# Performance work log

Hardware: AMD Instinct MI355X
Metric: run time of the kernel (lower is better)

The kernel has to match this reference:

```python
import jax, jax.numpy as jnp
import numpy as np

B, N, D = 32, 1024, 256

def setup_inputs() -> dict:
    key = jax.random.key(0)
    ks = jax.random.split(key, 7)
    s = 1.0 / np.sqrt(D)
    return {
        "traj": jax.random.normal(ks[0], (B, N, D), dtype=jnp.float32),
        "Wq": jax.random.normal(ks[1], (D, D), dtype=jnp.float32) * s,
        "bq": jax.random.normal(ks[2], (D,), dtype=jnp.float32) * s,
        "Wk": jax.random.normal(ks[3], (D, D), dtype=jnp.float32) * s,
        "bk": jax.random.normal(ks[4], (D,), dtype=jnp.float32) * s,
        "Wv": jax.random.normal(ks[5], (D, D), dtype=jnp.float32) * s,
        "bv": jax.random.normal(ks[6], (D,), dtype=jnp.float32) * s,
    }

def reference(traj, Wq, bq, Wk, bk, Wv, bv):
    # torch nn.Linear: y = x @ W.T + b
    q = jnp.einsum('bnd,ed->bne', traj, Wq) + bq  # [B,N,D]
    k = jnp.einsum('bnd,ed->bne', traj, Wk) + bk  # [B,N,D]
    v = jnp.einsum('bnd,ed->bne', traj, Wv) + bv  # [B,N,D]
    # unscaled dot-product attention (original sums broadcasted Q*K over D)
    scores = jnp.einsum('bnd,bmd->bnm', q, k)     # [B,N,N]
    attn = jax.nn.softmax(scores, axis=-1)        # [B,N,N]
    out = jnp.einsum('bnm,bmd->bnd', attn, v)     # [B,N,D]
    return out
```

## Files before the change

### kernel.cpp

```cpp
#include <hip/hip_runtime.h>

#define NN 1024
#define DD 256

typedef __attribute__((ext_vector_type(8))) _Float16 f16x8;
typedef __attribute__((ext_vector_type(4))) _Float16 f16x4;
typedef __attribute__((ext_vector_type(4))) float f32x4;

union H8 { f16x8 v; _Float16 s[8]; };

__device__ __forceinline__ void g2lds16(const void* g, void* l) {
  __builtin_amdgcn_global_load_lds(
      (const __attribute__((address_space(1))) void*)g,
      (__attribute__((address_space(3))) void*)l, 16, 0, 0);
}

__global__ void wconv_kernel(const float* __restrict__ Wq, const float* __restrict__ Wk,
                             const float* __restrict__ Wv, _Float16* __restrict__ pw) {
  int c = blockIdx.x * 256 + threadIdx.x;
  int lane = c & 63;
  int nt = (c >> 6) & 1;
  int kk = (c >> 7) & 7;
  int et = c >> 10;
  int e = et * 32 + nt * 16 + (lane & 15);
  int d = kk * 32 + (lane >> 4) * 8;
  const float* W = (e < 256) ? Wq : (e < 512 ? Wk : Wv);
  const float* src = W + (e & 255) * 256 + d;
  H8 xx;
  for (int j = 0; j < 8; ++j) xx.s[j] = (_Float16)src[j];
  *(f16x8*)(pw + (size_t)c * 8) = xx.v;
}

__global__ __launch_bounds__(256, 2) void proj_kernel(
    const float* __restrict__ traj,
    const float* __restrict__ bq, const float* __restrict__ bk, const float* __restrict__ bv,
    const _Float16* __restrict__ pw,
    _Float16* __restrict__ pq, _Float16* __restrict__ pk, _Float16* __restrict__ pv)
{
  __shared__ alignas(16) _Float16 Wl[2][8192];
  __shared__ alignas(16) _Float16 Cs[4][1280];

  const int t = threadIdx.x;
  const int lane = t & 63, wave = t >> 6;
  const int col16 = lane & 15, quad = lane >> 4;
  const int mt = blockIdx.x >> 1, eh = blockIdx.x & 1;
  const int mbase = mt * 128;
  const int bb = mbase >> 10;

  f16x8 aq[2][8];
  for (int s = 0; s < 2; ++s) {
    const float* ap = traj + (size_t)(mbase + wave * 32 + s * 16 + col16) * DD;
    for (int kk = 0; kk < 8; ++kk) {
      float4 u0 = *(const float4*)(ap + kk * 32 + quad * 8);
      float4 u1 = *(const float4*)(ap + kk * 32 + quad * 8 + 4);
      H8 xx;
      xx.s[0] = (_Float16)u0.x; xx.s[1] = (_Float16)u0.y;
      xx.s[2] = (_Float16)u0.z; xx.s[3] = (_Float16)u0.w;
      xx.s[4] = (_Float16)u1.x; xx.s[5] = (_Float16)u1.y;
      xx.s[6] = (_Float16)u1.z; xx.s[7] = (_Float16)u1.w;
      aq[s][kk] = xx.v;
    }
  }

  const f32x4 zero = {0.f, 0.f, 0.f, 0.f};
  const int et0 = eh * 12;

  for (int i = 0; i < 4; ++i)
    g2lds16(pw + (size_t)et0 * 8192 + (size_t)(i * 256 + t) * 8, Wl[0] + (i * 256 + t) * 8);
  for (int i = 0; i < 4; ++i)
    g2lds16(pw + (size_t)(et0 + 1) * 8192 + (size_t)(i * 256 + t) * 8, Wl[1] + (i * 256 + t) * 8);

  for (int ei = 0; ei < 12; ++ei) {
    if (ei == 0)      asm volatile("s_waitcnt vmcnt(4)" ::: "memory");
    else if (ei < 11) asm volatile("s_waitcnt vmcnt(6)" ::: "memory");
    else              asm volatile("s_waitcnt vmcnt(0)" ::: "memory");
    __builtin_amdgcn_s_barrier();
    asm volatile("" ::: "memory");

    const _Float16* wl = Wl[ei & 1];

    f32x4 acc[2][2];
    acc[0][0] = zero; acc[0][1] = zero; acc[1][0] = zero; acc[1][1] = zero;
    for (int kk = 0; kk < 8; ++kk)
      for (int nt = 0; nt < 2; ++nt) {
        f16x8 bw = *(const f16x8*)&wl[((kk * 2 + nt) * 64 + lane) * 8];
        acc[0][nt] = __builtin_amdgcn_mfma_f32_16x16x32_f16(aq[0][kk], bw, acc[0][nt], 0, 0, 0);
        acc[1][nt] = __builtin_amdgcn_mfma_f32_16x16x32_f16(aq[1][kk], bw, acc[1][nt], 0, 0, 0);
      }

    int e0 = eh * 384 + ei * 32;
    int sel = e0 >> 8;
    const float* bias = (sel == 0) ? bq : (sel == 1 ? bk : bv);
    for (int nt = 0; nt < 2; ++nt) {
      float bvl = bias[(e0 & 255) + nt * 16 + col16];
      for (int s = 0; s < 2; ++s) {
        acc[s][nt][0] += bvl; acc[s][nt][1] += bvl;
        acc[s][nt][2] += bvl; acc[s][nt][3] += bvl;
      }
    }

    _Float16* cs = Cs[wave];
    if (sel < 2) {
      for (int s = 0; s < 2; ++s)
        for (int nt = 0; nt < 2; ++nt)
          for (int r = 0; r < 4; ++r)
            cs[(s * 16 + quad * 4 + r) * 40 + nt * 16 + col16] = (_Float16)acc[s][nt][r];
      if (sel == 0) {
        for (int s = 0; s < 2; ++s) {
          f16x8 val = *(const f16x8*)&cs[(s * 16 + col16) * 40 + quad * 8];
          int g = (mbase >> 4) + wave * 2 + s;
          *(f16x8*)(pq + (size_t)((g * 8 + ei) * 64 + lane) * 8) = val;
        }
      } else {
        int kkg = (e0 - 256) >> 5;
        for (int s = 0; s < 2; ++s) {
          f16x8 val = *(const f16x8*)&cs[(s * 16 + col16) * 40 + quad * 8];
          int kgg = ((mbase & 1023) >> 4) + wave * 2 + s;
          *(f16x8*)(pk + (size_t)(((bb * 64 + kgg) * 8 + kkg) * 64 + lane) * 8) = val;
        }
      }
    } else {
      for (int s = 0; s < 2; ++s)
        for (int nt = 0; nt < 2; ++nt)
          for (int r = 0; r < 4; ++r)
            cs[(nt * 16 + col16) * 40 + s * 16 + quad * 4 + r] = (_Float16)acc[s][nt][r];
      int kt32 = ((mbase & 1023) >> 5) + wave;
      for (int dtl = 0; dtl < 2; ++dtl) {
        const _Float16* base = &cs[(dtl * 16 + col16) * 40];
        H8 val;
        *(f16x4*)&val.s[0] = *(const f16x4*)&base[quad * 4];
        *(f16x4*)&val.s[4] = *(const f16x4*)&base[16 + quad * 4];
        int dtg = ((e0 - 512) >> 4) + dtl;
        *(f16x8*)(pv + (size_t)(((bb * 32 + kt32) * 16 + dtg) * 64 + lane) * 8) = val.v;
      }
    }

    asm volatile("" ::: "memory");
    __builtin_amdgcn_s_barrier();
    if (ei < 10) {
      const _Float16* ws = pw + (size_t)(et0 + ei + 2) * 8192;
      _Float16* wd = Wl[ei & 1];
      for (int i = 0; i < 4; ++i)
        g2lds16(ws + (size_t)(i * 256 + t) * 8, wd + (i * 256 + t) * 8);
    }
  }
}

__global__ __launch_bounds__(256, 2) void attn_kernel(
    const _Float16* __restrict__ pq, const _Float16* __restrict__ pk,
    const _Float16* __restrict__ pv, float* __restrict__ out)
{
  __shared__ alignas(16) _Float16 Ks[2][8192];
  __shared__ alignas(16) _Float16 Vs[2][8192];

  const int t = threadIdx.x;
  const int lane = t & 63, wave = t >> 6;
  const int col16 = lane & 15, quad = lane >> 4;
  const int b = blockIdx.x, qt = blockIdx.y;
  const int qrow0 = b * NN + qt * 64;

  f16x8 aq[8];
  {
    int g = b * 64 + qt * 4 + wave;
#pragma unroll
    for (int kk = 0; kk < 8; ++kk)
      aq[kk] = *(const f16x8*)(pq + (size_t)((g * 8 + kk) * 64 + lane) * 8);
  }

  float m_i = -3.0e38f, l_i = 0.f;
  f32x4 O[16];
  const f32x4 zero = {0.f, 0.f, 0.f, 0.f};
#pragma unroll
  for (int dt = 0; dt < 16; ++dt) O[dt] = zero;

  const _Float16* kbb = pk + (size_t)b * 64 * 8 * 64 * 8;
  const _Float16* vbb = pv + (size_t)b * 32 * 16 * 64 * 8;

#pragma unroll
  for (int i = 0; i < 4; ++i) g2lds16(kbb + (size_t)(i * 256 + t) * 8, &Ks[0][(i * 256 + t) * 8]);
#pragma unroll
  for (int i = 0; i < 4; ++i) g2lds16(vbb + (size_t)(i * 256 + t) * 8, &Vs[0][(i * 256 + t) * 8]);
#pragma unroll
  for (int i = 0; i < 4; ++i) g2lds16(kbb + 8192 + (size_t)(i * 256 + t) * 8, &Ks[1][(i * 256 + t) * 8]);
#pragma unroll
  for (int i = 0; i < 4; ++i) g2lds16(vbb + 8192 + (size_t)(i * 256 + t) * 8, &Vs[1][(i * 256 + t) * 8]);

  for (int kt = 0; kt < 32; ++kt) {
    if (kt < 31) asm volatile("s_waitcnt vmcnt(8)" ::: "memory");
    else         asm volatile("s_waitcnt vmcnt(0)" ::: "memory");
    __builtin_amdgcn_s_barrier();
    asm volatile("" ::: "memory");

    const _Float16* ks = Ks[kt & 1];
    f32x4 S[2]; S[0] = zero; S[1] = zero;
    __builtin_amdgcn_s_setprio(1);
#pragma unroll
    for (int kk = 0; kk < 8; ++kk)
#pragma unroll
      for (int nt = 0; nt < 2; ++nt) {
        f16x8 bk_ = *(const f16x8*)&ks[((nt * 8 + kk) * 64 + lane) * 8];
        S[nt] = __builtin_amdgcn_mfma_f32_16x16x32_f16(bk_, aq[kk], S[nt], 0, 0, 0);
      }
    __builtin_amdgcn_s_setprio(0);

    float sv[8];
#pragma unroll
    for (int nt = 0; nt < 2; ++nt)
#pragma unroll
      for (int r = 0; r < 4; ++r) sv[nt * 4 + r] = S[nt][r];
    float vmax = sv[0];
#pragma unroll
    for (int j = 1; j < 8; ++j) vmax = fmaxf(vmax, sv[j]);
    vmax = fmaxf(vmax, __shfl_xor(vmax, 16));
    vmax = fmaxf(vmax, __shfl_xor(vmax, 32));

    if (__ballot(vmax > m_i + 8.0f)) {
      float nm = fmaxf(m_i, vmax);
      float alpha = __expf(m_i - nm);
      float a4[4];
#pragma unroll
      for (int r = 0; r < 4; ++r) a4[r] = __shfl(alpha, quad * 4 + r);
#pragma unroll
      for (int dt = 0; dt < 16; ++dt)
#pragma unroll
        for (int r = 0; r < 4; ++r) O[dt][r] *= a4[r];
      l_i *= alpha;
      m_i = nm;
    }
    float rs = 0.f;
    H8 px;
#pragma unroll
    for (int j = 0; j < 8; ++j) {
      float pj = __expf(sv[j] - m_i);
      rs += pj;
      px.s[j] = (_Float16)pj;
    }
    rs += __shfl_xor(rs, 16);
    rs += __shfl_xor(rs, 32);
    l_i += rs;
    f16x8 ap = px.v;

    const _Float16* vs = Vs[kt & 1];
    __builtin_amdgcn_s_setprio(1);
#pragma unroll
    for (int dt = 0; dt < 16; ++dt) {
      f16x8 bv_ = *(const f16x8*)&vs[(dt * 64 + lane) * 8];
      O[dt] = __builtin_amdgcn_mfma_f32_16x16x32_f16(ap, bv_, O[dt], 0, 0, 0);
    }
    __builtin_amdgcn_s_setprio(0);

    asm volatile("" ::: "memory");
    __builtin_amdgcn_s_barrier();
    if (kt < 30) {
      const _Float16* kg = kbb + (size_t)(kt + 2) * 8192;
      const _Float16* vg = vbb + (size_t)(kt + 2) * 8192;
      _Float16* kd = Ks[kt & 1];
      _Float16* vd = Vs[kt & 1];
#pragma unroll
      for (int i = 0; i < 4; ++i) g2lds16(kg + (size_t)(i * 256 + t) * 8, kd + (i * 256 + t) * 8);
#pragma unroll
      for (int i = 0; i < 4; ++i) g2lds16(vg + (size_t)(i * 256 + t) * 8, vd + (i * 256 + t) * 8);
    }
  }

  float linv[4];
#pragma unroll
  for (int r = 0; r < 4; ++r) linv[r] = 1.0f / __shfl(l_i, quad * 4 + r);
#pragma unroll
  for (int r = 0; r < 4; ++r) {
    float* orow = out + (size_t)(qrow0 + wave * 16 + quad * 4 + r) * DD;
#pragma unroll
    for (int dt = 0; dt < 16; ++dt)
      orow[dt * 16 + col16] = O[dt][r] * linv[r];
  }
}

extern "C" void kernel_launch(void* const* d_in, const int* in_sizes, int n_in,
                              void* d_out, int out_size, void* d_ws, size_t ws_size,
                              hipStream_t stream) {
  const float* traj = (const float*)d_in[0];
  const float* Wq   = (const float*)d_in[1];
  const float* bq   = (const float*)d_in[2];
  const float* Wk   = (const float*)d_in[3];
  const float* bk   = (const float*)d_in[4];
  const float* Wv   = (const float*)d_in[5];
  const float* bv   = (const float*)d_in[6];

  _Float16* pq = (_Float16*)d_ws;
  _Float16* pk = pq + (size_t)32768 * 256;
  _Float16* pv = pk + (size_t)32768 * 256;
  _Float16* pw = pv + (size_t)32768 * 256;

  wconv_kernel<<<96, 256, 0, stream>>>(Wq, Wk, Wv, pw);
  proj_kernel<<<512, 256, 0, stream>>>(traj, bq, bk, bv, pw, pq, pk, pv);
  attn_kernel<<<dim3(32, 16), 256, 0, stream>>>(pq, pk, pv, (float*)d_out);
}
```

Measured before the change: 165.0 us.

## Software-pipeline QK^T one tile ahead of softmax and PV in attention loop

The main attention loop now computes the QK^T scores for tile kt while running softmax and the PV product for tile kt-1, using a prologue and an epilogue. K tiles are prefetched two tiles ahead and V tiles one tile ahead, with the vmcnt waits adjusted to match. The goal is to hide softmax latency, such as exp and cross-lane shuffles, behind independent MFMA work. The cost is extra registers for the carried score tile and more complex buffer indexing and wait counts.

```diff
diff --git a/kernel.cpp b/kernel.cpp
--- a/kernel.cpp
+++ b/kernel.cpp
@@ -182,24 +182,47 @@
   for (int i = 0; i < 4; ++i) g2lds16(vbb + (size_t)(i * 256 + t) * 8, &Vs[0][(i * 256 + t) * 8]);
 #pragma unroll
   for (int i = 0; i < 4; ++i) g2lds16(kbb + 8192 + (size_t)(i * 256 + t) * 8, &Ks[1][(i * 256 + t) * 8]);
-#pragma unroll
-  for (int i = 0; i < 4; ++i) g2lds16(vbb + 8192 + (size_t)(i * 256 + t) * 8, &Vs[1][(i * 256 + t) * 8]);
-
-  for (int kt = 0; kt < 32; ++kt) {
+
+  asm volatile("s_waitcnt vmcnt(8)" ::: "memory");
+  __builtin_amdgcn_s_barrier();
+  asm volatile("" ::: "memory");
+
+  f32x4 Sp[2]; Sp[0] = zero; Sp[1] = zero;
+  {
+    const _Float16* ks = Ks[0];
+    __builtin_amdgcn_s_setprio(1);
+#pragma unroll
+    for (int kk = 0; kk < 8; ++kk)
+#pragma unroll
+      for (int nt = 0; nt < 2; ++nt) {
+        f16x8 bk_ = *(const f16x8*)&ks[((nt * 8 + kk) * 64 + lane) * 8];
+        Sp[nt] = __builtin_amdgcn_mfma_f32_16x16x32_f16(bk_, aq[kk], Sp[nt], 0, 0, 0);
+      }
+    __builtin_amdgcn_s_setprio(0);
+  }
+
+  asm volatile("" ::: "memory");
+  __builtin_amdgcn_s_barrier();
+#pragma unroll
+  for (int i = 0; i < 4; ++i) g2lds16(kbb + 2 * 8192 + (size_t)(i * 256 + t) * 8, &Ks[0][(i * 256 + t) * 8]);
+#pragma unroll
+  for (int i = 0; i < 4; ++i) g2lds16(vbb + 1 * 8192 + (size_t)(i * 256 + t) * 8, &Vs[1][(i * 256 + t) * 8]);
+
+  for (int kt = 1; kt < 32; ++kt) {
     if (kt < 31) asm volatile("s_waitcnt vmcnt(8)" ::: "memory");
-    else         asm volatile("s_waitcnt vmcnt(0)" ::: "memory");
+    else         asm volatile("s_waitcnt vmcnt(4)" ::: "memory");
     __builtin_amdgcn_s_barrier();
     asm volatile("" ::: "memory");
 
     const _Float16* ks = Ks[kt & 1];
-    f32x4 S[2]; S[0] = zero; S[1] = zero;
+    f32x4 Sc[2]; Sc[0] = zero; Sc[1] = zero;
     __builtin_amdgcn_s_setprio(1);
 #pragma unroll
     for (int kk = 0; kk < 8; ++kk)
 #pragma unroll
       for (int nt = 0; nt < 2; ++nt) {
         f16x8 bk_ = *(const f16x8*)&ks[((nt * 8 + kk) * 64 + lane) * 8];
-        S[nt] = __builtin_amdgcn_mfma_f32_16x16x32_f16(bk_, aq[kk], S[nt], 0, 0, 0);
+        Sc[nt] = __builtin_amdgcn_mfma_f32_16x16x32_f16(bk_, aq[kk], Sc[nt], 0, 0, 0);
       }
     __builtin_amdgcn_s_setprio(0);
 
@@ -207,13 +230,12 @@
 #pragma unroll
     for (int nt = 0; nt < 2; ++nt)
 #pragma unroll
-      for (int r = 0; r < 4; ++r) sv[nt * 4 + r] = S[nt][r];
+      for (int r = 0; r < 4; ++r) sv[nt * 4 + r] = Sp[nt][r];
     float vmax = sv[0];
 #pragma unroll
     for (int j = 1; j < 8; ++j) vmax = fmaxf(vmax, sv[j]);
     vmax = fmaxf(vmax, __shfl_xor(vmax, 16));
     vmax = fmaxf(vmax, __shfl_xor(vmax, 32));
-
     if (__ballot(vmax > m_i + 8.0f)) {
       float nm = fmaxf(m_i, vmax);
       float alpha = __expf(m_i - nm);
@@ -240,7 +262,7 @@
     l_i += rs;
     f16x8 ap = px.v;
 
-    const _Float16* vs = Vs[kt & 1];
+    const _Float16* vs = Vs[(kt - 1) & 1];
     __builtin_amdgcn_s_setprio(1);
 #pragma unroll
     for (int dt = 0; dt < 16; ++dt) {
@@ -251,16 +273,68 @@
 
     asm volatile("" ::: "memory");
     __builtin_amdgcn_s_barrier();
-    if (kt < 30) {
+    if (kt <= 29) {
       const _Float16* kg = kbb + (size_t)(kt + 2) * 8192;
-      const _Float16* vg = vbb + (size_t)(kt + 2) * 8192;
       _Float16* kd = Ks[kt & 1];
-      _Float16* vd = Vs[kt & 1];
 #pragma unroll
       for (int i = 0; i < 4; ++i) g2lds16(kg + (size_t)(i * 256 + t) * 8, kd + (i * 256 + t) * 8);
+    }
+    if (kt <= 30) {
+      const _Float16* vg = vbb + (size_t)(kt + 1) * 8192;
+      _Float16* vd = Vs[(kt + 1) & 1];
 #pragma unroll
       for (int i = 0; i < 4; ++i) g2lds16(vg + (size_t)(i * 256 + t) * 8, vd + (i * 256 + t) * 8);
     }
+    Sp[0] = Sc[0]; Sp[1] = Sc[1];
+  }
+
+  asm volatile("s_waitcnt vmcnt(0)" ::: "memory");
+  __builtin_amdgcn_s_barrier();
+  asm volatile("" ::: "memory");
+  {
+    float sv[8];
+#pragma unroll
+    for (int nt = 0; nt < 2; ++nt)
+#pragma unroll
+      for (int r = 0; r < 4; ++r) sv[nt * 4 + r] = Sp[nt][r];
+    float vmax = sv[0];
+#pragma unroll
+    for (int j = 1; j < 8; ++j) vmax = fmaxf(vmax, sv[j]);
+    vmax = fmaxf(vmax, __shfl_xor(vmax, 16));
+    vmax = fmaxf(vmax, __shfl_xor(vmax, 32));
+    if (__ballot(vmax > m_i + 8.0f)) {
+      float nm = fmaxf(m_i, vmax);
+      float alpha = __expf(m_i - nm);
+      float a4[4];
+#pragma unroll
+      for (int r = 0; r < 4; ++r) a4[r] = __shfl(alpha, quad * 4 + r);
+#pragma unroll
+      for (int dt = 0; dt < 16; ++dt)
+#pragma unroll
+        for (int r = 0; r < 4; ++r) O[dt][r] *= a4[r];
+      l_i *= alpha;
+      m_i = nm;
+    }
+    float rs = 0.f;
+    H8 px;
+#pragma unroll
+    for (int j = 0; j < 8; ++j) {
+      float pj = __expf(sv[j] - m_i);
+      rs += pj;
+      px.s[j] = (_Float16)pj;
+    }
+    rs += __shfl_xor(rs, 16);
+    rs += __shfl_xor(rs, 32);
+    l_i += rs;
+    f16x8 ap = px.v;
+    const _Float16* vs = Vs[1];
+    __builtin_amdgcn_s_setprio(1);
+#pragma unroll
+    for (int dt = 0; dt < 16; ++dt) {
+      f16x8 bv_ = *(const f16x8*)&vs[(dt * 64 + lane) * 8];
+      O[dt] = __builtin_amdgcn_mfma_f32_16x16x32_f16(ap, bv_, O[dt], 0, 0, 0);
+    }
+    __builtin_amdgcn_s_setprio(0);
   }
 
   float linv[4];
```

After: 164.5 us, median of 2. Within noise of the previous version (-0.3%).

## Single-buffer V in LDS via register staging and raise occupancy bound

Applied to the files above, without the earlier changes.

The V tile is no longer double-buffered in LDS. The next V tile is loaded into registers at the top of each iteration and written to a single LDS buffer after the PV MFMAs, guarded by an extra lgkmcnt wait and barrier. This cuts LDS per block to 48KB so the launch bound can go from 2 to 3 blocks per CU. The cost is a second barrier per iteration, more live registers that cap the VGPR budget, and V loads that are no longer asynchronous. With 512 blocks on 256 CUs the extra occupancy slot may go unused.

```diff
diff --git a/kernel.cpp b/kernel.cpp
--- a/kernel.cpp
+++ b/kernel.cpp
@@ -146,12 +146,12 @@
   }
 }
 
-__global__ __launch_bounds__(256, 2) void attn_kernel(
+__global__ __launch_bounds__(256, 3) void attn_kernel(
     const _Float16* __restrict__ pq, const _Float16* __restrict__ pk,
     const _Float16* __restrict__ pv, float* __restrict__ out)
 {
   __shared__ alignas(16) _Float16 Ks[2][8192];
-  __shared__ alignas(16) _Float16 Vs[2][8192];
+  __shared__ alignas(16) _Float16 Vs[8192];
 
   const int t = threadIdx.x;
   const int lane = t & 63, wave = t >> 6;
@@ -178,18 +178,29 @@
 
 #pragma unroll
   for (int i = 0; i < 4; ++i) g2lds16(kbb + (size_t)(i * 256 + t) * 8, &Ks[0][(i * 256 + t) * 8]);
-#pragma unroll
-  for (int i = 0; i < 4; ++i) g2lds16(vbb + (size_t)(i * 256 + t) * 8, &Vs[0][(i * 256 + t) * 8]);
+  float4 vr0, vr1, vr2, vr3;
+  {
+    const float4* vgp = (const float4*)vbb;
+    vr0 = vgp[0 * 256 + t]; vr1 = vgp[1 * 256 + t];
+    vr2 = vgp[2 * 256 + t]; vr3 = vgp[3 * 256 + t];
+  }
 #pragma unroll
   for (int i = 0; i < 4; ++i) g2lds16(kbb + 8192 + (size_t)(i * 256 + t) * 8, &Ks[1][(i * 256 + t) * 8]);
-#pragma unroll
-  for (int i = 0; i < 4; ++i) g2lds16(vbb + 8192 + (size_t)(i * 256 + t) * 8, &Vs[1][(i * 256 + t) * 8]);
+  {
+    float4* vsp = (float4*)Vs;
+    vsp[0 * 256 + t] = vr0; vsp[1 * 256 + t] = vr1;
+    vsp[2 * 256 + t] = vr2; vsp[3 * 256 + t] = vr3;
+  }
+  asm volatile("s_waitcnt lgkmcnt(0)" ::: "memory");
+  __builtin_amdgcn_s_barrier();
+  asm volatile("" ::: "memory");
 
   for (int kt = 0; kt < 32; ++kt) {
-    if (kt < 31) asm volatile("s_waitcnt vmcnt(8)" ::: "memory");
-    else         asm volatile("s_waitcnt vmcnt(0)" ::: "memory");
-    __builtin_amdgcn_s_barrier();
-    asm volatile("" ::: "memory");
+    if (kt < 31) {
+      const float4* vgp = (const float4*)(vbb + (size_t)(kt + 1) * 8192);
+      vr0 = vgp[0 * 256 + t]; vr1 = vgp[1 * 256 + t];
+      vr2 = vgp[2 * 256 + t]; vr3 = vgp[3 * 256 + t];
+    }
 
     const _Float16* ks = Ks[kt & 1];
     f32x4 S[2]; S[0] = zero; S[1] = zero;
@@ -240,27 +251,32 @@
     l_i += rs;
     f16x8 ap = px.v;
 
-    const _Float16* vs = Vs[kt & 1];
     __builtin_amdgcn_s_setprio(1);
 #pragma unroll
     for (int dt = 0; dt < 16; ++dt) {
-      f16x8 bv_ = *(const f16x8*)&vs[(dt * 64 + lane) * 8];
+      f16x8 bv_ = *(const f16x8*)&Vs[(dt * 64 + lane) * 8];
       O[dt] = __builtin_amdgcn_mfma_f32_16x16x32_f16(ap, bv_, O[dt], 0, 0, 0);
     }
     __builtin_amdgcn_s_setprio(0);
 
     asm volatile("" ::: "memory");
     __builtin_amdgcn_s_barrier();
+    asm volatile("" ::: "memory");
+
+    if (kt < 31) {
+      float4* vsp = (float4*)Vs;
+      vsp[0 * 256 + t] = vr0; vsp[1 * 256 + t] = vr1;
+      vsp[2 * 256 + t] = vr2; vsp[3 * 256 + t] = vr3;
+    }
     if (kt < 30) {
       const _Float16* kg = kbb + (size_t)(kt + 2) * 8192;
-      const _Float16* vg = vbb + (size_t)(kt + 2) * 8192;
       _Float16* kd = Ks[kt & 1];
-      _Float16* vd = Vs[kt & 1];
 #pragma unroll
       for (int i = 0; i < 4; ++i) g2lds16(kg + (size_t)(i * 256 + t) * 8, kd + (i * 256 + t) * 8);
-#pragma unroll
-      for (int i = 0; i < 4; ++i) g2lds16(vg + (size_t)(i * 256 + t) * 8, vd + (i * 256 + t) * 8);
-    }
+    }
+    asm volatile("s_waitcnt lgkmcnt(0)" ::: "memory");
+    __builtin_amdgcn_s_barrier();
+    asm volatile("" ::: "memory");
   }
 
   float linv[4];
```

Measured after the change: 167.8 us. About the same (+1.7%).
